# Performance work log

Hardware: AMD Instinct MI355X
Metric: run time of the kernel (lower is better)

## Reference

```python
import jax, jax.numpy as jnp
import numpy as np

EPS = 1e-12  # torch F.normalize eps

def _l2norm(x, axis):
    n = jnp.sqrt(jnp.sum(x * x, axis=axis, keepdims=True))
    return x / jnp.maximum(n, EPS)

def setup_inputs() -> dict:
    key = jax.random.key(0)
    k1, k2, k3, k4 = jax.random.split(key, 4)
    B, D, Hc, Wc = 2, 256, 60, 80
    DESC = jax.random.normal(k1, (B, D, Hc, Wc), jnp.float32)
    warp_DESC = jax.random.normal(k2, (B, D, Hc, Wc), jnp.float32)
    eye = jnp.broadcast_to(jnp.eye(3, dtype=jnp.float32), (B, 3, 3))
    H = eye + 0.01 * jax.random.normal(k3, (B, 3, 3), jnp.float32)
    H_invert = eye + 0.01 * jax.random.normal(k4, (B, 3, 3), jnp.float32)
    v_mask = jnp.ones((B, 1, Hc * 8, Wc * 8), jnp.float32)
    return {"DESC": DESC, "warp_DESC": warp_DESC, "H": H, "H_invert": H_invert, "v_mask": v_mask}

def reference(DESC, warp_DESC, H, H_invert, v_mask):
    B, D, Hc, Wc = DESC.shape
    # cell-center coordinates (y, x), stride 8, offset 4
    ys, xs = jnp.meshgrid(jnp.arange(Hc, dtype=jnp.float32), jnp.arange(Wc, dtype=jnp.float32), indexing='ij')
    cords = jnp.stack([ys, xs], axis=-1) * 8.0 + 4.0  # [Hc, Wc, 2] (y, x)
    # warp (x, y, 1) by H_invert (kornia warp_grid = perspective transform)
    pts = jnp.stack([cords[..., 1], cords[..., 0], jnp.ones((Hc, Wc), jnp.float32)], axis=-1)  # [Hc,Wc,3]
    q = jnp.einsum('bij,hwj->bhwi', H_invert, pts)  # [B,Hc,Wc,3]
    z = q[..., 2:3]
    z = jnp.where(jnp.abs(z) > 1e-8, z, 1e-8)
    xy_warp = q[..., :2] / z                      # (x', y')
    warp_cords = xy_warp[..., ::-1]               # (y', x')  [B,Hc,Wc,2]
    # S[b,h,w,h',w'] = 1 if warped (h,w) is within 7.5 px of (h',w')
    diff = cords[None, None, None, :, :, :] - warp_cords[:, :, :, None, None, :]
    dist = jnp.sqrt(jnp.sum(diff * diff, axis=-1))  # [B,Hc,Wc,Hc,Wc]
    S = (dist <= 7.5).astype(jnp.float32)
    # NOTE: the original uses .view on [B,D,Hc,Wc] (a raw reshape, not permute);
    # we replicate that exactly for faithfulness.
    desc = _l2norm(DESC.reshape(B, Hc, Wc, D), axis=-1)
    warp_desc = _l2norm(warp_DESC.reshape(B, Hc, Wc, D), axis=-1)
    dot = jnp.einsum('bijd,bkld->bijkl', desc, warp_desc)  # [B,Hc,Wc,Hc,Wc]
    dot = jax.nn.relu(dot)
    dot = _l2norm(dot.reshape(B, Hc, Wc, Hc * Wc), axis=3).reshape(B, Hc, Wc, Hc, Wc)
    dot = _l2norm(dot.reshape(B, Hc * Wc, Hc, Wc), axis=1).reshape(B, Hc, Wc, Hc, Wc)
    pos_margin, neg_margin, lambda_d = 1.0, 0.2, 250.0
    positive_dist = jnp.maximum(0.0, pos_margin - dot)
    negative_dist = jnp.maximum(0.0, dot - neg_margin)
    loss = lambda_d * S * positive_dist + (1.0 - S) * negative_dist
    # per-8x8-block validity: product of mask values in each block
    blocks = v_mask[:, 0].reshape(B, Hc, 8, Wc, 8)
    valid = jnp.prod(blocks, axis=(2, 4))  # [B,Hc,Wc]
    valid5 = valid[:, None, None, :, :]    # [B,1,1,Hc,Wc]
    normalization = jnp.sum(valid, axis=(1, 2)) * (Hc * Wc)  # [B]
    per_batch = jnp.sum(loss * valid5, axis=(1, 2, 3, 4)) / normalization
    return jnp.sum(per_batch)
```

## Files before the change

### kernel.cpp

```cpp
#include <hip/hip_runtime.h>

#define HC 60
#define WC 80
#define NPTS 4800
#define DD 256
#define MP 4864
#define NB 2
#define NPART 1600

typedef __attribute__((ext_vector_type(8))) short short8;
typedef __attribute__((ext_vector_type(4))) float f32x4;
typedef __bf16 bf16x8 __attribute__((ext_vector_type(8)));

__device__ __forceinline__ float bf2f(unsigned short u) {
  unsigned x = ((unsigned)u) << 16;
  return __builtin_bit_cast(float, x);
}
__device__ __forceinline__ unsigned short f2bf(float f) {
  unsigned u = __builtin_bit_cast(unsigned, f);
  u += 0x7fffu + ((u >> 16) & 1u);
  return (unsigned short)(u >> 16);
}

__global__ void init_kernel(float* __restrict__ C2, float* __restrict__ R2,
                            float* __restrict__ normsum, float* __restrict__ out,
                            const float* __restrict__ Hinv, float* __restrict__ wc) {
  int idx = blockIdx.x * 256 + threadIdx.x;
  if (idx < NB) normsum[idx] = 0.f;
  if (idx == 0) out[0] = 0.f;
  if (idx >= NB * NPTS) return;
  C2[idx] = 0.f; R2[idx] = 0.f;
  int b = idx / NPTS, r = idx % NPTS;
  int i = r / WC, j = r % WC;
  float y = i * 8.f + 4.f, x = j * 8.f + 4.f;
  const float* h = Hinv + b * 9;
  float q0 = h[0] * x + h[1] * y + h[2];
  float q1 = h[3] * x + h[4] * y + h[5];
  float z  = h[6] * x + h[7] * y + h[8];
  if (fabsf(z) <= 1e-8f) z = 1e-8f;
  wc[idx * 2 + 0] = q1 / z;
  wc[idx * 2 + 1] = q0 / z;
}

__global__ void prep_kernel(const float* __restrict__ din, const float* __restrict__ win,
                            unsigned short* __restrict__ dN, unsigned short* __restrict__ wN) {
  const int r = blockIdx.x;
  const int b = blockIdx.y;
  const int which = blockIdx.z;
  const float* src = which ? win : din;
  unsigned short* dst = which ? wN : dN;
  const int t = threadIdx.x;
  const size_t oo = ((size_t)b * MP + r) * DD + t;
  if (r >= NPTS) { dst[oo] = 0; return; }
  const float v = src[((size_t)b * NPTS + r) * DD + t];
  float s = v * v;
#pragma unroll
  for (int o = 32; o; o >>= 1) s += __shfl_xor(s, o, 64);
  __shared__ float red[4];
  if ((t & 63) == 0) red[t >> 6] = s;
  __syncthreads();
  const float tot = red[0] + red[1] + red[2] + red[3];
  const float scale = 1.f / fmaxf(sqrtf(tot), 1e-12f);
  dst[oo] = f2bf(v * scale);
}

__global__ void valid_kernel(const float* __restrict__ vmask, float* __restrict__ valid) {
  int gid = blockIdx.x * 256 + threadIdx.x;
  int cell = gid >> 5;
  int tt = gid & 31;
  if (cell >= NB * NPTS) return;
  int b = cell / NPTS, kl = cell % NPTS;
  int k = kl / WC, l = kl % WC;
  const float* base = vmask + (size_t)b * (NPTS * 64) + (size_t)(k * 8) * (WC * 8) + l * 8;
  int e = tt * 2;
  float p = base[(e >> 3) * (WC * 8) + (e & 7)] * base[((e + 1) >> 3) * (WC * 8) + ((e + 1) & 7)];
#pragma unroll
  for (int o = 16; o; o >>= 1) p *= __shfl_xor(p, o, 32);
  if (tt == 0) valid[cell] = p;
}

__global__ __launch_bounds__(256, 2)
void gemm_kernel(const unsigned short* __restrict__ A,
                 const unsigned short* __restrict__ Bm,
                 unsigned short* __restrict__ dot, float* __restrict__ R2) {
  __shared__ unsigned short As[128 * 64];
  __shared__ unsigned short Bs[128 * 64];
  const int bi = blockIdx.x;
  const int bj = blockIdx.y;
  const int b  = blockIdx.z;
  const int t = threadIdx.x;
  const int lane = t & 63;
  const int w = t >> 6;
  const int wr = w >> 1, wc = w & 1;
  const int ls = lane >> 3;
  const int swz = (lane & 7) ^ ls;
  const int l15 = lane & 15, g4 = lane >> 4;

  const unsigned short* Ab = A + ((size_t)b * MP + (size_t)bj * 128) * DD;
  const unsigned short* Bb = Bm + ((size_t)b * MP + (size_t)bi * 128) * DD;

  f32x4 acc[4][4] = {};

  for (int k0 = 0; k0 < DD; k0 += 64) {
#pragma unroll
    for (int s = 0; s < 4; ++s) {
      int row = w * 8 + s * 32 + ls;
      const unsigned short* gA = Ab + row * DD + k0 + swz * 8;
      const unsigned short* gB = Bb + row * DD + k0 + swz * 8;
      __builtin_amdgcn_global_load_lds(
          (__attribute__((address_space(1))) unsigned int*)(size_t)gA,
          (__attribute__((address_space(3))) unsigned int*)((char*)As + w * 1024 + s * 4096),
          16, 0, 0);
      __builtin_amdgcn_global_load_lds(
          (__attribute__((address_space(1))) unsigned int*)(size_t)gB,
          (__attribute__((address_space(3))) unsigned int*)((char*)Bs + w * 1024 + s * 4096),
          16, 0, 0);
    }
    __syncthreads();
#pragma unroll
    for (int kk = 0; kk < 2; ++kk) {
      short8 af[4], bfr[4];
#pragma unroll
      for (int m = 0; m < 4; ++m) {
        int row = wr * 64 + m * 16 + l15;
        int colb = (kk * 64 + g4 * 16) ^ ((row & 7) << 4);
        af[m] = *(const short8*)((const char*)As + row * 128 + colb);
      }
#pragma unroll
      for (int n = 0; n < 4; ++n) {
        int row = wc * 64 + n * 16 + l15;
        int colb = (kk * 64 + g4 * 16) ^ ((row & 7) << 4);
        bfr[n] = *(const short8*)((const char*)Bs + row * 128 + colb);
      }
#pragma unroll
      for (int m = 0; m < 4; ++m)
#pragma unroll
        for (int n = 0; n < 4; ++n)
          acc[m][n] = __builtin_amdgcn_mfma_f32_16x16x32_bf16(
              __builtin_bit_cast(bf16x8, af[m]),
              __builtin_bit_cast(bf16x8, bfr[n]),
              acc[m][n], 0, 0, 0);
    }
    __syncthreads();
  }

#pragma unroll
  for (int m = 0; m < 4; ++m) {
#pragma unroll
    for (int r = 0; r < 4; ++r) {
      const int grow = bj * 128 + wr * 64 + m * 16 + g4 * 4 + r;
      const size_t base = ((size_t)b * NPTS + grow) * NPTS;
      float rs = 0.f;
#pragma unroll
      for (int n = 0; n < 4; ++n) {
        const float v = fmaxf(acc[m][n][r], 0.f);
        rs += v * v;
        const int gcol = bi * 128 + wc * 64 + n * 16 + l15;
        if (grow < NPTS && gcol < NPTS) dot[base + gcol] = f2bf(v);
      }
#pragma unroll
      for (int o = 1; o < 16; o <<= 1) rs += __shfl_xor(rs, o, 64);
      if (l15 == 0 && grow < NPTS)
        atomicAdd(&R2[(size_t)b * NPTS + grow], rs);
    }
  }
}

__global__ void invr_kernel(float* __restrict__ R2, const float* __restrict__ valid,
                            float* __restrict__ normsum) {
  const int t = threadIdx.x;
  const int i = blockIdx.x * 256 + t;
  float v0 = 0.f, v1 = 0.f;
  if (i < NB * NPTS) {
    R2[i] = 1.f / fmaxf(sqrtf(R2[i]), 1e-12f);
    const float v = valid[i];
    if (i < NPTS) v0 = v; else v1 = v;
  }
#pragma unroll
  for (int o = 32; o; o >>= 1) { v0 += __shfl_xor(v0, o, 64); v1 += __shfl_xor(v1, o, 64); }
  __shared__ float r0[4], r1[4];
  if ((t & 63) == 0) { r0[t >> 6] = v0; r1[t >> 6] = v1; }
  __syncthreads();
  if (t == 0) {
    const float s0 = r0[0] + r0[1] + r0[2] + r0[3];
    const float s1 = r1[0] + r1[1] + r1[2] + r1[3];
    if (s0 != 0.f) atomicAdd(&normsum[0], s0);
    if (s1 != 0.f) atomicAdd(&normsum[1], s1);
  }
}

__global__ void colsum_kernel(const unsigned short* __restrict__ dot,
                              const float* __restrict__ invR, float* __restrict__ C2) {
  const int p = blockIdx.x * 256 + threadIdx.x;
  if (p >= NPTS / 2) return;
  const int rc = blockIdx.y, b = blockIdx.z;
  const int r0 = rc * 60;
  float s0 = 0.f, s1 = 0.f;
  for (int r = r0; r < r0 + 60; ++r) {
    const size_t ro = (size_t)b * NPTS + r;
    const unsigned u = *(const unsigned*)(dot + ro * NPTS + p * 2);
    const float ir = invR[ro];
    const float f0 = __builtin_bit_cast(float, u << 16) * ir;
    const float f1 = __builtin_bit_cast(float, u & 0xffff0000u) * ir;
    s0 += f0 * f0; s1 += f1 * f1;
  }
  atomicAdd(&C2[b * NPTS + p * 2], s0);
  atomicAdd(&C2[b * NPTS + p * 2 + 1], s1);
}

__global__ void loss_kernel(const unsigned short* __restrict__ dot,
                            const float* __restrict__ invR, const float* __restrict__ C2,
                            const float* __restrict__ valid, const float* __restrict__ normsum,
                            const float* __restrict__ wc, float* __restrict__ partial) {
  const int t = threadIdx.x;
  const int p = blockIdx.x * 256 + t;
  const int rc = blockIdx.y, b = blockIdx.z;
  float acc = 0.f;
  if (p < NPTS / 2) {
    const int c0 = p * 2;
    const float invC0 = 1.f / fmaxf(sqrtf(C2[b * NPTS + c0]), 1e-12f);
    const float invC1 = 1.f / fmaxf(sqrtf(C2[b * NPTS + c0 + 1]), 1e-12f);
    const float yk  = (float)(c0 / WC) * 8.f + 4.f;
    const float xl0 = (float)(c0 % WC) * 8.f + 4.f;
    const float xl1 = xl0 + 8.f;
    const int r0 = rc * 60;
    float a0 = 0.f, a1 = 0.f;
    for (int r = r0; r < r0 + 60; ++r) {
      const size_t ro = (size_t)b * NPTS + r;
      const unsigned u = *(const unsigned*)(dot + ro * NPTS + c0);
      const float ir = invR[ro];
      const float d0 = __builtin_bit_cast(float, u << 16) * ir * invC0;
      const float d1 = __builtin_bit_cast(float, u & 0xffff0000u) * ir * invC1;
      const float wy = wc[ro * 2 + 0], wx = wc[ro * 2 + 1];
      const float dy = yk - wy, dx0 = xl0 - wx, dx1 = xl1 - wx;
      const bool S0 = (dy * dy + dx0 * dx0) <= 56.25f;
      const bool S1 = (dy * dy + dx1 * dx1) <= 56.25f;
      a0 += S0 ? 250.f * fmaxf(0.f, 1.f - d0) : fmaxf(0.f, d0 - 0.2f);
      a1 += S1 ? 250.f * fmaxf(0.f, 1.f - d1) : fmaxf(0.f, d1 - 0.2f);
    }
    acc = (a0 * valid[b * NPTS + c0] + a1 * valid[b * NPTS + c0 + 1])
          / (normsum[b] * (float)NPTS);
  }
#pragma unroll
  for (int o = 32; o; o >>= 1) acc += __shfl_xor(acc, o, 64);
  __shared__ float red[4];
  if ((t & 63) == 0) red[t >> 6] = acc;
  __syncthreads();
  if (t == 0)
    partial[blockIdx.x + 10 * (blockIdx.y + 80 * blockIdx.z)] =
        red[0] + red[1] + red[2] + red[3];
}

__global__ void final_kernel(const float* __restrict__ partial, float* __restrict__ out) {
  const int t = threadIdx.x;
  float s = 0.f;
  for (int i = t; i < NPART; i += 256) s += partial[i];
#pragma unroll
  for (int o = 32; o; o >>= 1) s += __shfl_xor(s, o, 64);
  __shared__ float red[4];
  if ((t & 63) == 0) red[t >> 6] = s;
  __syncthreads();
  if (t == 0) out[0] = red[0] + red[1] + red[2] + red[3];
}

extern "C" void kernel_launch(void* const* d_in, const int* in_sizes, int n_in,
                              void* d_out, int out_size, void* d_ws, size_t ws_size,
                              hipStream_t stream) {
  (void)in_sizes; (void)n_in; (void)out_size; (void)ws_size;
  const float* DESC  = (const float*)d_in[0];
  const float* WDESC = (const float*)d_in[1];
  const float* HINV  = (const float*)d_in[3];
  const float* VMASK = (const float*)d_in[4];
  float* out = (float*)d_out;

  char* p = (char*)d_ws;
  auto take = [&](size_t bytes) { char* q = p; p += (bytes + 255) & ~(size_t)255; return q; };
  unsigned short* dN   = (unsigned short*)take((size_t)NB * MP * DD * 2);
  unsigned short* wN   = (unsigned short*)take((size_t)NB * MP * DD * 2);
  unsigned short* dotb = (unsigned short*)take((size_t)NB * NPTS * NPTS * 2);
  float* R2      = (float*)take((size_t)NB * NPTS * 4);
  float* C2      = (float*)take((size_t)NB * NPTS * 4);
  float* validb  = (float*)take((size_t)NB * NPTS * 4);
  float* wcb     = (float*)take((size_t)NB * NPTS * 8);
  float* normsum = (float*)take(64);
  float* partial = (float*)take((size_t)NPART * 4);

  init_kernel  <<<dim3(38),          dim3(256), 0, stream>>>(C2, R2, normsum, out, HINV, wcb);
  prep_kernel  <<<dim3(MP, NB, 2),   dim3(256), 0, stream>>>(DESC, WDESC, dN, wN);
  valid_kernel <<<dim3(1200),        dim3(256), 0, stream>>>(VMASK, validb);
  gemm_kernel  <<<dim3(38, 38, NB),  dim3(256), 0, stream>>>(dN, wN, dotb, R2);
  invr_kernel  <<<dim3(38),          dim3(256), 0, stream>>>(R2, validb, normsum);
  colsum_kernel<<<dim3(10, 80, NB),  dim3(256), 0, stream>>>(dotb, R2, C2);
  loss_kernel  <<<dim3(10, 80, NB),  dim3(256), 0, stream>>>(dotb, R2, C2, validb, normsum, wcb, partial);
  final_kernel <<<dim3(1),           dim3(256), 0, stream>>>(partial, out);
}
```

Measured before the change: 194.4 us.

## Store dot matrix as custom FP8 and double-buffer GEMM LDS tiles

The GEMM epilogue quantizes the relu'd similarity values to a custom 8-bit float format (4-bit exponent, 3-bit mantissa with subnormals) instead of bf16. The row norms are accumulated from the quantized values to stay consistent. The colsum and loss kernels are rewritten to read four FP8 values per 32-bit load. The GEMM K loop gains double-buffered LDS staging so the next tile's global loads overlap with MFMA compute. The aim is to halve the traffic for the large intermediate matrix, at the cost of reduced precision near the loss margins.

```diff
diff --git a/kernel.cpp b/kernel.cpp
--- a/kernel.cpp
+++ b/kernel.cpp
@@ -6,20 +6,29 @@
 #define DD 256
 #define MP 4864
 #define NB 2
-#define NPART 1600
+#define NPART 800
 
 typedef __attribute__((ext_vector_type(8))) short short8;
 typedef __attribute__((ext_vector_type(4))) float f32x4;
 typedef __bf16 bf16x8 __attribute__((ext_vector_type(8)));
 
-__device__ __forceinline__ float bf2f(unsigned short u) {
-  unsigned x = ((unsigned)u) << 16;
-  return __builtin_bit_cast(float, x);
-}
 __device__ __forceinline__ unsigned short f2bf(float f) {
   unsigned u = __builtin_bit_cast(unsigned, f);
   u += 0x7fffu + ((u >> 16) & 1u);
   return (unsigned short)(u >> 16);
+}
+
+__device__ __forceinline__ unsigned fp8e(float x) {
+  unsigned sub = (unsigned)rintf(x * 512.f);
+  unsigned u = __builtin_bit_cast(unsigned, x);
+  u += 0x7FFFFu + ((u >> 20) & 1u);
+  unsigned nrm = (((u >> 23) - 120u) << 3) | ((u >> 20) & 7u);
+  return x < 0.015625f ? sub : nrm;
+}
+__device__ __forceinline__ float fp8d(unsigned c) {
+  unsigned e = (c >> 3) & 15u, m = c & 7u;
+  float nrm = __builtin_bit_cast(float, ((e + 120u) << 23) | (m << 20));
+  return e ? nrm : (float)m * 0.001953125f;
 }
 
 __global__ void init_kernel(float* __restrict__ C2, float* __restrict__ R2,
@@ -79,12 +88,12 @@
   if (tt == 0) valid[cell] = p;
 }
 
-__global__ __launch_bounds__(256, 2)
+__global__ __launch_bounds__(256)
 void gemm_kernel(const unsigned short* __restrict__ A,
                  const unsigned short* __restrict__ Bm,
-                 unsigned short* __restrict__ dot, float* __restrict__ R2) {
-  __shared__ unsigned short As[128 * 64];
-  __shared__ unsigned short Bs[128 * 64];
+                 unsigned char* __restrict__ dot, float* __restrict__ R2) {
+  __shared__ unsigned short As[2][128 * 64];
+  __shared__ unsigned short Bs[2][128 * 64];
   const int bi = blockIdx.x;
   const int bj = blockIdx.y;
   const int b  = blockIdx.z;
@@ -101,7 +110,7 @@
 
   f32x4 acc[4][4] = {};
 
-  for (int k0 = 0; k0 < DD; k0 += 64) {
+  auto stage = [&](int buf, int k0) {
 #pragma unroll
     for (int s = 0; s < 4; ++s) {
       int row = w * 8 + s * 32 + ls;
@@ -109,14 +118,16 @@
       const unsigned short* gB = Bb + row * DD + k0 + swz * 8;
       __builtin_amdgcn_global_load_lds(
           (__attribute__((address_space(1))) unsigned int*)(size_t)gA,
-          (__attribute__((address_space(3))) unsigned int*)((char*)As + w * 1024 + s * 4096),
+          (__attribute__((address_space(3))) unsigned int*)((char*)&As[buf][0] + w * 1024 + s * 4096),
           16, 0, 0);
       __builtin_amdgcn_global_load_lds(
           (__attribute__((address_space(1))) unsigned int*)(size_t)gB,
-          (__attribute__((address_space(3))) unsigned int*)((char*)Bs + w * 1024 + s * 4096),
+          (__attribute__((address_space(3))) unsigned int*)((char*)&Bs[buf][0] + w * 1024 + s * 4096),
           16, 0, 0);
     }
-    __syncthreads();
+  };
+
+  auto compute = [&](int buf) {
 #pragma unroll
     for (int kk = 0; kk < 2; ++kk) {
       short8 af[4], bfr[4];
@@ -124,13 +135,13 @@
       for (int m = 0; m < 4; ++m) {
         int row = wr * 64 + m * 16 + l15;
         int colb = (kk * 64 + g4 * 16) ^ ((row & 7) << 4);
-        af[m] = *(const short8*)((const char*)As + row * 128 + colb);
+        af[m] = *(const short8*)((const char*)&As[buf][0] + row * 128 + colb);
       }
 #pragma unroll
       for (int n = 0; n < 4; ++n) {
         int row = wc * 64 + n * 16 + l15;
         int colb = (kk * 64 + g4 * 16) ^ ((row & 7) << 4);
-        bfr[n] = *(const short8*)((const char*)Bs + row * 128 + colb);
+        bfr[n] = *(const short8*)((const char*)&Bs[buf][0] + row * 128 + colb);
       }
 #pragma unroll
       for (int m = 0; m < 4; ++m)
@@ -141,8 +152,19 @@
               __builtin_bit_cast(bf16x8, bfr[n]),
               acc[m][n], 0, 0, 0);
     }
+  };
+
+  stage(0, 0);
+  asm volatile("s_waitcnt vmcnt(0)" ::: "memory");
+  __syncthreads();
+#pragma unroll
+  for (int it = 0; it < 3; ++it) {
+    stage((it + 1) & 1, (it + 1) * 64);
+    compute(it & 1);
+    asm volatile("s_waitcnt vmcnt(0)" ::: "memory");
     __syncthreads();
   }
+  compute(1);
 
 #pragma unroll
   for (int m = 0; m < 4; ++m) {
@@ -154,9 +176,11 @@
 #pragma unroll
       for (int n = 0; n < 4; ++n) {
         const float v = fmaxf(acc[m][n][r], 0.f);
-        rs += v * v;
+        const unsigned q = fp8e(v);
+        const float vq = fp8d(q);
+        rs += vq * vq;
         const int gcol = bi * 128 + wc * 64 + n * 16 + l15;
-        if (grow < NPTS && gcol < NPTS) dot[base + gcol] = f2bf(v);
+        if (grow < NPTS && gcol < NPTS) dot[base + gcol] = (unsigned char)q;
       }
 #pragma unroll
       for (int o = 1; o < 16; o <<= 1) rs += __shfl_xor(rs, o, 64);
@@ -189,26 +213,30 @@
   }
 }
 
-__global__ void colsum_kernel(const unsigned short* __restrict__ dot,
+__global__ void colsum_kernel(const unsigned char* __restrict__ dot,
                               const float* __restrict__ invR, float* __restrict__ C2) {
   const int p = blockIdx.x * 256 + threadIdx.x;
-  if (p >= NPTS / 2) return;
+  if (p >= NPTS / 4) return;
   const int rc = blockIdx.y, b = blockIdx.z;
   const int r0 = rc * 60;
-  float s0 = 0.f, s1 = 0.f;
+  float s0 = 0.f, s1 = 0.f, s2 = 0.f, s3 = 0.f;
   for (int r = r0; r < r0 + 60; ++r) {
     const size_t ro = (size_t)b * NPTS + r;
-    const unsigned u = *(const unsigned*)(dot + ro * NPTS + p * 2);
+    const unsigned u = *(const unsigned*)(dot + ro * NPTS + p * 4);
     const float ir = invR[ro];
-    const float f0 = __builtin_bit_cast(float, u << 16) * ir;
-    const float f1 = __builtin_bit_cast(float, u & 0xffff0000u) * ir;
-    s0 += f0 * f0; s1 += f1 * f1;
-  }
-  atomicAdd(&C2[b * NPTS + p * 2], s0);
-  atomicAdd(&C2[b * NPTS + p * 2 + 1], s1);
-}
-
-__global__ void loss_kernel(const unsigned short* __restrict__ dot,
+    const float f0 = fp8d(u & 255u) * ir;
+    const float f1 = fp8d((u >> 8) & 255u) * ir;
+    const float f2 = fp8d((u >> 16) & 255u) * ir;
+    const float f3 = fp8d(u >> 24) * ir;
+    s0 += f0 * f0; s1 += f1 * f1; s2 += f2 * f2; s3 += f3 * f3;
+  }
+  atomicAdd(&C2[b * NPTS + p * 4 + 0], s0);
+  atomicAdd(&C2[b * NPTS + p * 4 + 1], s1);
+  atomicAdd(&C2[b * NPTS + p * 4 + 2], s2);
+  atomicAdd(&C2[b * NPTS + p * 4 + 3], s3);
+}
+
+__global__ void loss_kernel(const unsigned char* __restrict__ dot,
                             const float* __restrict__ invR, const float* __restrict__ C2,
                             const float* __restrict__ valid, const float* __restrict__ normsum,
                             const float* __restrict__ wc, float* __restrict__ partial) {
@@ -216,30 +244,36 @@
   const int p = blockIdx.x * 256 + t;
   const int rc = blockIdx.y, b = blockIdx.z;
   float acc = 0.f;
-  if (p < NPTS / 2) {
-    const int c0 = p * 2;
-    const float invC0 = 1.f / fmaxf(sqrtf(C2[b * NPTS + c0]), 1e-12f);
-    const float invC1 = 1.f / fmaxf(sqrtf(C2[b * NPTS + c0 + 1]), 1e-12f);
+  if (p < NPTS / 4) {
+    const int c0 = p * 4;
+    float invC[4], xl[4];
+#pragma unroll
+    for (int n = 0; n < 4; ++n)
+      invC[n] = 1.f / fmaxf(sqrtf(C2[b * NPTS + c0 + n]), 1e-12f);
     const float yk  = (float)(c0 / WC) * 8.f + 4.f;
-    const float xl0 = (float)(c0 % WC) * 8.f + 4.f;
-    const float xl1 = xl0 + 8.f;
+    const float x0  = (float)(c0 % WC) * 8.f + 4.f;
+#pragma unroll
+    for (int n = 0; n < 4; ++n) xl[n] = x0 + 8.f * n;
     const int r0 = rc * 60;
-    float a0 = 0.f, a1 = 0.f;
+    float a[4] = {0.f, 0.f, 0.f, 0.f};
     for (int r = r0; r < r0 + 60; ++r) {
       const size_t ro = (size_t)b * NPTS + r;
       const unsigned u = *(const unsigned*)(dot + ro * NPTS + c0);
       const float ir = invR[ro];
-      const float d0 = __builtin_bit_cast(float, u << 16) * ir * invC0;
-      const float d1 = __builtin_bit_cast(float, u & 0xffff0000u) * ir * invC1;
       const float wy = wc[ro * 2 + 0], wx = wc[ro * 2 + 1];
-      const float dy = yk - wy, dx0 = xl0 - wx, dx1 = xl1 - wx;
-      const bool S0 = (dy * dy + dx0 * dx0) <= 56.25f;
-      const bool S1 = (dy * dy + dx1 * dx1) <= 56.25f;
-      a0 += S0 ? 250.f * fmaxf(0.f, 1.f - d0) : fmaxf(0.f, d0 - 0.2f);
-      a1 += S1 ? 250.f * fmaxf(0.f, 1.f - d1) : fmaxf(0.f, d1 - 0.2f);
+      const float dy2 = (yk - wy) * (yk - wy);
+#pragma unroll
+      for (int n = 0; n < 4; ++n) {
+        const float d = fp8d((u >> (8 * n)) & 255u) * ir * invC[n];
+        const float dx = xl[n] - wx;
+        const bool S = (dy2 + dx * dx) <= 56.25f;
+        a[n] += S ? 250.f * fmaxf(0.f, 1.f - d) : fmaxf(0.f, d - 0.2f);
+      }
     }
-    acc = (a0 * valid[b * NPTS + c0] + a1 * valid[b * NPTS + c0 + 1])
-          / (normsum[b] * (float)NPTS);
+    float num = 0.f;
+#pragma unroll
+    for (int n = 0; n < 4; ++n) num += a[n] * valid[b * NPTS + c0 + n];
+    acc = num / (normsum[b] * (float)NPTS);
   }
 #pragma unroll
   for (int o = 32; o; o >>= 1) acc += __shfl_xor(acc, o, 64);
@@ -247,7 +281,7 @@
   if ((t & 63) == 0) red[t >> 6] = acc;
   __syncthreads();
   if (t == 0)
-    partial[blockIdx.x + 10 * (blockIdx.y + 80 * blockIdx.z)] =
+    partial[blockIdx.x + 5 * (blockIdx.y + 80 * blockIdx.z)] =
         red[0] + red[1] + red[2] + red[3];
 }
 
@@ -275,9 +309,9 @@
 
   char* p = (char*)d_ws;
   auto take = [&](size_t bytes) { char* q = p; p += (bytes + 255) & ~(size_t)255; return q; };
-  unsigned short* dN   = (unsigned short*)take((size_t)NB * MP * DD * 2);
-  unsigned short* wN   = (unsigned short*)take((size_t)NB * MP * DD * 2);
-  unsigned short* dotb = (unsigned short*)take((size_t)NB * NPTS * NPTS * 2);
+  unsigned short* dN  = (unsigned short*)take((size_t)NB * MP * DD * 2);
+  unsigned short* wN  = (unsigned short*)take((size_t)NB * MP * DD * 2);
+  unsigned char* dotb = (unsigned char*)take((size_t)NB * NPTS * NPTS);
   float* R2      = (float*)take((size_t)NB * NPTS * 4);
   float* C2      = (float*)take((size_t)NB * NPTS * 4);
   float* validb  = (float*)take((size_t)NB * NPTS * 4);
@@ -290,7 +324,7 @@
   valid_kernel <<<dim3(1200),        dim3(256), 0, stream>>>(VMASK, validb);
   gemm_kernel  <<<dim3(38, 38, NB),  dim3(256), 0, stream>>>(dN, wN, dotb, R2);
   invr_kernel  <<<dim3(38),          dim3(256), 0, stream>>>(R2, validb, normsum);
-  colsum_kernel<<<dim3(10, 80, NB),  dim3(256), 0, stream>>>(dotb, R2, C2);
-  loss_kernel  <<<dim3(10, 80, NB),  dim3(256), 0, stream>>>(dotb, R2, C2, validb, normsum, wcb, partial);
+  colsum_kernel<<<dim3(5, 80, NB),   dim3(256), 0, stream>>>(dotb, R2, C2);
+  loss_kernel  <<<dim3(5, 80, NB),   dim3(256), 0, stream>>>(dotb, R2, C2, validb, normsum, wcb, partial);
   final_kernel <<<dim3(1),           dim3(256), 0, stream>>>(partial, out);
 }
```

Result: slower. 250.7 us (+29.0%).
